# Kernel optimization log

Measured on AMD Instinct MI355X. Metric: run time of the kernel, lower is better.

## Reference

```python
import jax, jax.numpy as jnp
import numpy as np

BETA = 0.25
B, N, D = 8, 4096, 256
NUM_CODES = 4096


def setup_inputs() -> dict:
    key = jax.random.key(0)
    kx, kc = jax.random.split(key)
    x = jax.random.normal(kx, (B, N, D), dtype=jnp.float32)
    # matches nn.init.uniform_(weight, -1/dim, 1/dim)
    codebook = jax.random.uniform(kc, (NUM_CODES, D), dtype=jnp.float32,
                                  minval=-1.0 / D, maxval=1.0 / D)
    return {"x": x, "codebook": codebook}


def reference(x, codebook):
    b, n, d = x.shape
    flat = x.reshape(b * n, d)                                   # [BN, D]
    # squared euclidean distances: ||z||^2 - 2 z.e^T + ||e||^2   # [BN, K]
    distances = (jnp.sum(flat * flat, axis=1, keepdims=True)
                 - 2.0 * jnp.einsum('md,kd->mk', flat, codebook)
                 + jnp.sum(codebook * codebook, axis=1)[None, :])
    indices = jnp.argmin(distances, axis=1)                      # [BN]
    z_q = codebook[indices].reshape(b, n, d)                     # [B, N, D]
    # commitment + codebook losses (detach == stop_gradient)
    sg = jax.lax.stop_gradient
    loss = jnp.mean((sg(z_q) - x) ** 2) + BETA * jnp.mean((z_q - sg(x)) ** 2)
    # straight-through estimator
    z_q_st = x + sg(z_q - x)
    return z_q_st, loss, indices.reshape(b, n)
```

## Files before the change

kernel.cpp:

```cpp
#include <hip/hip_runtime.h>

#define MTOT 32768
#define KC   4096
#define DDIM 256
#define BM   128
#define ZELEMS (MTOT * DDIM)
#define THRESH 2.0e-4f
#define WLCAP 8192
#define RGRID 2048

typedef _Float16 half8 __attribute__((ext_vector_type(8)));
typedef float f32x4 __attribute__((ext_vector_type(4)));

__device__ __forceinline__ void gload_lds16(const void* g, void* l) {
  __builtin_amdgcn_global_load_lds(
      (const __attribute__((address_space(1))) void*)g,
      (__attribute__((address_space(3))) void*)l, 16, 0, 0);
}

__device__ __forceinline__ float sqr_rn(float v) { return __fmul_rn(v, v); }

__global__ __launch_bounds__(256) void vq_prep2(const float* __restrict__ x,
                                                const float* __restrict__ cb,
                                                float* __restrict__ S,
                                                float* __restrict__ cnorm,
                                                _Float16* __restrict__ cbsw,
                                                int* __restrict__ wl_count,
                                                double* __restrict__ accum) {
  const int t = threadIdx.x;
  if (blockIdx.x == 0 && t == 0) { *accum = 0.0; *wl_count = 0; }
  const int sub = t >> 4, lane16 = t & 15;
  const int h = lane16 >> 3, j = lane16 & 7;
  const bool isrow = blockIdx.x < 2048;
  const int idx = (isrow ? blockIdx.x : blockIdx.x - 2048) * 16 + sub;
  const float* p = (isrow ? x + (size_t)idx * DDIM : cb + (size_t)idx * DDIM);

  float r = 0.f;
  const float* q = p + h * 128 + j;
#pragma unroll
  for (int i = 0; i < 16; ++i) r = __fadd_rn(r, sqr_rn(q[i * 8]));
  r = __fadd_rn(r, __shfl_xor(r, 1, 64));
  r = __fadd_rn(r, __shfl_xor(r, 2, 64));
  r = __fadd_rn(r, __shfl_xor(r, 4, 64));
  float sv = __fadd_rn(r, __shfl_xor(r, 8, 64));
  if (lane16 == 0) {
    if (isrow) S[idx] = sv; else cnorm[idx] = sv;
  }

  if (!isrow) {
    const int sw = idx & 7;
    _Float16* dst = cbsw + (size_t)idx * DDIM;
#pragma unroll
    for (int c = 0; c < 2; ++c) {
      int jj = lane16 + c * 16;
      float4 a4 = *reinterpret_cast<const float4*>(p + jj * 8);
      float4 b4 = *reinterpret_cast<const float4*>(p + jj * 8 + 4);
      union { half8 v; _Float16 hh[8]; } u;
      u.hh[0] = (_Float16)(a4.x * 256.0f); u.hh[1] = (_Float16)(a4.y * 256.0f);
      u.hh[2] = (_Float16)(a4.z * 256.0f); u.hh[3] = (_Float16)(a4.w * 256.0f);
      u.hh[4] = (_Float16)(b4.x * 256.0f); u.hh[5] = (_Float16)(b4.y * 256.0f);
      u.hh[6] = (_Float16)(b4.z * 256.0f); u.hh[7] = (_Float16)(b4.w * 256.0f);
      *reinterpret_cast<half8*>(dst + ((jj ^ sw) * 8)) = u.v;
    }
  }
}

__global__ __launch_bounds__(512, 2) void vq_score(const float* __restrict__ x,
                                                   const _Float16* __restrict__ cbsw,
                                                   const float* __restrict__ Sarr,
                                                   const float* __restrict__ cnorm,
                                                   int* __restrict__ bestidx,
                                                   int* __restrict__ wl,
                                                   int* __restrict__ wl_count,
                                                   double* __restrict__ accum) {
  __shared__ _Float16 cbt[2][64 * DDIM];
  __shared__ float cn[KC];
  __shared__ float scrV1[4][BM];
  __shared__ float scrV2[4][BM];
  __shared__ int   scrI1[4][BM];
  __shared__ float wred[8];

  const int t = threadIdx.x;
  const int m0 = blockIdx.x * BM;
  const int lane = t & 63, w = t >> 6;
  const int rg = w >> 2, cg = w & 3;
  const int lo = lane & 15, hi = lane >> 4;

#pragma unroll
  for (int j = 0; j < 4; ++j)
    gload_lds16(cbsw + 0 * 16384 + w * 2048 + j * 512 + lane * 8,
                &cbt[0][w * 2048 + j * 512]);
#pragma unroll
  for (int j = 0; j < 4; ++j)
    gload_lds16(cbsw + 1 * 16384 + w * 2048 + j * 512 + lane * 8,
                &cbt[1][w * 2048 + j * 512]);

#pragma unroll
  for (int i = 0; i < 2; ++i) {
    int fi = t + i * 512;
    *reinterpret_cast<float4*>(&cn[fi * 4]) =
        *reinterpret_cast<const float4*>(cnorm + fi * 4);
  }

  half8 a[4][8];
#pragma unroll
  for (int s2 = 0; s2 < 4; ++s2) {
    const float* xr = x + (size_t)(m0 + rg * 64 + s2 * 16 + lo) * DDIM + hi * 8;
#pragma unroll
    for (int s = 0; s < 8; ++s) {
      float4 u0 = *reinterpret_cast<const float4*>(xr + s * 32);
      float4 u1 = *reinterpret_cast<const float4*>(xr + s * 32 + 4);
      union { half8 v; _Float16 h[8]; } uu;
      uu.h[0] = (_Float16)u0.x; uu.h[1] = (_Float16)u0.y;
      uu.h[2] = (_Float16)u0.z; uu.h[3] = (_Float16)u0.w;
      uu.h[4] = (_Float16)u1.x; uu.h[5] = (_Float16)u1.y;
      uu.h[6] = (_Float16)u1.z; uu.h[7] = (_Float16)u1.w;
      a[s2][s] = uu.v;
    }
  }

  const int code_l = cg * 16 + lo;
  const int bswz = (lo & 7) << 3;

  float v1[4][4], v2[4][4]; int i1[4][4];
#pragma unroll
  for (int s2 = 0; s2 < 4; ++s2)
#pragma unroll
    for (int r = 0; r < 4; ++r) { v1[s2][r] = 3.4e38f; v2[s2][r] = 3.4e38f; i1[s2][r] = 0; }

  __syncthreads();

  for (int kt = 0; kt < KC / 64; ++kt) {
    const int cur = kt & 1;
    if (kt < KC / 64 - 1) asm volatile("s_waitcnt vmcnt(4)" ::: "memory");
    else                  asm volatile("s_waitcnt vmcnt(0)" ::: "memory");
    __builtin_amdgcn_s_barrier();

    const float C = cn[kt * 64 + code_l];
    f32x4 acc[4];
#pragma unroll
    for (int s2 = 0; s2 < 4; ++s2) acc[s2] = (f32x4){0.f, 0.f, 0.f, 0.f};
#pragma unroll
    for (int s = 0; s < 8; ++s) {
      half8 b = *reinterpret_cast<half8*>(
          &cbt[cur][(code_l * DDIM + s * 32 + hi * 8) ^ bswz]);
      acc[0] = __builtin_amdgcn_mfma_f32_16x16x32_f16(a[0][s], b, acc[0], 0, 0, 0);
      acc[1] = __builtin_amdgcn_mfma_f32_16x16x32_f16(a[1][s], b, acc[1], 0, 0, 0);
      acc[2] = __builtin_amdgcn_mfma_f32_16x16x32_f16(a[2][s], b, acc[2], 0, 0, 0);
      acc[3] = __builtin_amdgcn_mfma_f32_16x16x32_f16(a[3][s], b, acc[3], 0, 0, 0);
    }
    const int code = kt * 64 + code_l;
#pragma unroll
    for (int s2 = 0; s2 < 4; ++s2) {
#pragma unroll
      for (int r = 0; r < 4; ++r) {
        float sv = fmaf(acc[s2][r], -0.0078125f, C);
        float mx = fmaxf(v1[s2][r], sv);
        v2[s2][r] = fminf(v2[s2][r], mx);
        bool lt = sv < v1[s2][r];
        if (lt) { v1[s2][r] = sv; i1[s2][r] = code; }
      }
    }

    __builtin_amdgcn_s_barrier();
    if (kt < KC / 64 - 2) {
#pragma unroll
      for (int j = 0; j < 4; ++j)
        gload_lds16(cbsw + (size_t)(kt + 2) * 16384 + w * 2048 + j * 512 + lane * 8,
                    &cbt[cur][w * 2048 + j * 512]);
    }
  }

#pragma unroll
  for (int s2 = 0; s2 < 4; ++s2) {
#pragma unroll
    for (int r = 0; r < 4; ++r) {
      float v = v1[s2][r], u = v2[s2][r]; int ii = i1[s2][r];
#pragma unroll
      for (int m = 1; m <= 8; m <<= 1) {
        float ov = __shfl_xor(v, m, 64);
        int   oi = __shfl_xor(ii, m, 64);
        float ou = __shfl_xor(u, m, 64);
        float mx = fmaxf(v, ov);
        u = fminf(fminf(u, ou), mx);
        bool take = (ov < v) || (ov == v && oi < ii);
        if (take) { v = ov; ii = oi; }
      }
      if (lo == 0) {
        int rowl = rg * 64 + s2 * 16 + hi * 4 + r;
        scrV1[cg][rowl] = v;
        scrV2[cg][rowl] = u;
        scrI1[cg][rowl] = ii;
      }
    }
  }
  __syncthreads();

  float part = 0.f;
  if (t < BM) {
    float bv1 = 3.4e38f, bv2 = 3.4e38f; int bi1 = 0x7fffffff;
#pragma unroll
    for (int c = 0; c < 4; ++c) {
      float v = scrV1[c][t];
      float u = scrV2[c][t];
      int  ii = scrI1[c][t];
      float mx = fmaxf(bv1, v);
      bv2 = fminf(fminf(bv2, u), mx);
      if (v < bv1 || (v == bv1 && ii < bi1)) { bv1 = v; bi1 = ii; }
    }
    int row = m0 + t;
    bestidx[row] = bi1;
    float gap = bv2 - bv1;
    if (gap <= THRESH) {
      int pos = atomicAdd(wl_count, 1);
      if (pos >= WLCAP) part = __fadd_rn(Sarr[row], bv1);
      else wl[pos] = row;
    } else {
      part = __fadd_rn(Sarr[row], bv1);
    }
  }
#pragma unroll
  for (int off = 32; off >= 1; off >>= 1) part += __shfl_down(part, off, 64);
  if (lane == 0) wred[w] = part;
  __syncthreads();
  if (t == 0) {
    double s = 0.0;
#pragma unroll
    for (int i = 0; i < 8; ++i) s += (double)wred[i];
    atomicAdd(accum, s);
  }
}

__global__ __launch_bounds__(256) void vq_rescore(const float* __restrict__ x,
                                                  const float* __restrict__ cb,
                                                  const float* __restrict__ Sarr,
                                                  const float* __restrict__ cnorm,
                                                  const int* __restrict__ wl,
                                                  const int* __restrict__ wl_count,
                                                  float* __restrict__ pD,
                                                  int* __restrict__ pI) {
  const int cnt = min(*wl_count, WLCAP);
  if (cnt == 0) return;
  const int ngroups = (cnt + 3) >> 2;
  const int nitems = ngroups * 16;

  __shared__ float xs[4][260];
  __shared__ int rsh[4];
  __shared__ float scrv[4][4];
  __shared__ int   scri[4][4];

  const int t = threadIdx.x;
  const int lane = t & 63, w = t >> 6;

  for (int item = blockIdx.x; item < nitems; item += RGRID) {
    const int g = item >> 4, chunk = item & 15;
    __syncthreads();
    if (t < 4) { int e = g * 4 + t; rsh[t] = wl[(e < cnt) ? e : g * 4]; }
    __syncthreads();
    { int i = t >> 6, dq = t & 63;
      *reinterpret_cast<float4*>(&xs[i][dq * 4]) =
          *reinterpret_cast<const float4*>(x + (size_t)rsh[i] * DDIM + dq * 4); }
    __syncthreads();

    const int code = chunk * 256 + t;
    const float* cp = cb + (size_t)code * DDIM;
    const float C = cnorm[code];

    float acc[4][4];
#pragma unroll
    for (int i = 0; i < 4; ++i)
#pragma unroll
      for (int l = 0; l < 4; ++l) acc[i][l] = 0.f;

#pragma unroll 8
    for (int dq = 0; dq < 64; ++dq) {
      float4 cv = *reinterpret_cast<const float4*>(cp + dq * 4);
#pragma unroll
      for (int i = 0; i < 4; ++i) {
        float4 xv = *reinterpret_cast<float4*>(&xs[i][dq * 4]);
        acc[i][0] = __fadd_rn(acc[i][0], __fmul_rn(xv.x, cv.x));
        acc[i][1] = __fadd_rn(acc[i][1], __fmul_rn(xv.y, cv.y));
        acc[i][2] = __fadd_rn(acc[i][2], __fmul_rn(xv.z, cv.z));
        acc[i][3] = __fadd_rn(acc[i][3], __fmul_rn(xv.w, cv.w));
      }
    }

#pragma unroll
    for (int i = 0; i < 4; ++i) {
      float e = __fadd_rn(__fadd_rn(acc[i][0], acc[i][1]),
                          __fadd_rn(acc[i][2], acc[i][3]));
      float Sv = Sarr[rsh[i]];
      float D = __fadd_rn(__fsub_rn(Sv, __fmul_rn(2.0f, e)), C);
      float v = D; int ii = code;
#pragma unroll
      for (int m = 1; m <= 32; m <<= 1) {
        float ov = __shfl_xor(v, m, 64);
        int   oi = __shfl_xor(ii, m, 64);
        if (ov < v || (ov == v && oi < ii)) { v = ov; ii = oi; }
      }
      if (lane == 0) { scrv[i][w] = v; scri[i][w] = ii; }
    }
    __syncthreads();
    if (t < 4) {
      float bv = 3.4e38f; int bi = 0x7fffffff;
#pragma unroll
      for (int c = 0; c < 4; ++c) {
        float v = scrv[t][c]; int ii = scri[t][c];
        if (v < bv || (v == bv && ii < bi)) { bv = v; bi = ii; }
      }
      int rpos = g * 4 + t;
      if (rpos < cnt) { pD[rpos * 16 + chunk] = bv; pI[rpos * 16 + chunk] = bi; }
    }
  }
}

__global__ __launch_bounds__(256) void vq_combine(const int* __restrict__ wl,
                                                  const int* __restrict__ wl_count,
                                                  const float* __restrict__ pD,
                                                  const int* __restrict__ pI,
                                                  int* __restrict__ bestidx,
                                                  double* __restrict__ accum) {
  const int cnt = min(*wl_count, WLCAP);
  for (int r = blockIdx.x * 256 + threadIdx.x; r < cnt; r += gridDim.x * 256) {
    float bv = 3.4e38f; int bi = 0x7fffffff;
#pragma unroll
    for (int c = 0; c < 16; ++c) {
      float v = pD[r * 16 + c]; int ii = pI[r * 16 + c];
      if (v < bv || (v == bv && ii < bi)) { bv = v; bi = ii; }
    }
    bestidx[wl[r]] = bi;
    atomicAdd(accum, (double)bv);
  }
}

__global__ __launch_bounds__(256) void vq_emit(const float* __restrict__ x,
                                               const float* __restrict__ cb,
                                               const int* __restrict__ bestidx,
                                               float* __restrict__ out) {
  __shared__ int ish[64];
  const int t = threadIdx.x;
  const int m0 = blockIdx.x * 64;
  if (t < 64) {
    int ii = bestidx[m0 + t];
    ish[t] = ii;
    out[(size_t)ZELEMS + 1 + m0 + t] = (float)ii;
  }
  __syncthreads();
#pragma unroll
  for (int i = 0; i < 16; ++i) {
    int fi = t + i * 256;
    int row = fi >> 6, dc = fi & 63;
    int code = ish[row];
    float4 c4 = *reinterpret_cast<const float4*>(cb + (size_t)code * DDIM + dc * 4);
    float4 x4 = *reinterpret_cast<const float4*>(x + (size_t)(m0 + row) * DDIM + dc * 4);
    float4 o;
    o.x = __fadd_rn(x4.x, __fsub_rn(c4.x, x4.x));
    o.y = __fadd_rn(x4.y, __fsub_rn(c4.y, x4.y));
    o.z = __fadd_rn(x4.z, __fsub_rn(c4.z, x4.z));
    o.w = __fadd_rn(x4.w, __fsub_rn(c4.w, x4.w));
    *reinterpret_cast<float4*>(out + (size_t)(m0 + row) * DDIM + dc * 4) = o;
  }
}

__global__ void vq_final(const double* __restrict__ accum, float* __restrict__ out) {
  out[ZELEMS] = (float)(1.25 * accum[0] / (double)ZELEMS);
}

extern "C" void kernel_launch(void* const* d_in, const int* in_sizes, int n_in,
                              void* d_out, int out_size, void* d_ws, size_t ws_size,
                              hipStream_t stream) {
  const float* x  = (const float*)d_in[0];
  const float* cb = (const float*)d_in[1];
  float* out = (float*)d_out;

  char* ws = (char*)d_ws;
  float*     S        = (float*)(ws + 0);
  float*     cnorm    = (float*)(ws + 131072);
  int*       bestidx  = (int*)  (ws + 147456);
  int*       wl       = (int*)  (ws + 278528);
  int*       wl_count = (int*)  (ws + 311296);
  double*    accum    = (double*)(ws + 311312);
  float*     pD       = (float*)(ws + 315392);
  int*       pI       = (int*)  (ws + 839680);
  _Float16*  cbsw     = (_Float16*)(ws + 1363968);

  vq_prep2<<<2304, 256, 0, stream>>>(x, cb, S, cnorm, cbsw, wl_count, accum);
  vq_score<<<MTOT / BM, 512, 0, stream>>>(x, cbsw, S, cnorm, bestidx, wl, wl_count, accum);
  vq_rescore<<<RGRID, 256, 0, stream>>>(x, cb, S, cnorm, wl, wl_count, pD, pI);
  vq_combine<<<8, 256, 0, stream>>>(wl, wl_count, pD, pI, bestidx, accum);
  vq_emit<<<MTOT / 64, 256, 0, stream>>>(x, cb, bestidx, out);
  vq_final<<<1, 1, 0, stream>>>(accum, out);
}
```

Baseline: 176.8 us.

## Deepen codebook LDS pipeline to four buffers, two tiles per barrier

```diff
diff --git a/kernel.cpp b/kernel.cpp
--- a/kernel.cpp
+++ b/kernel.cpp
@@ -65,7 +65,7 @@
   }
 }
 
-__global__ __launch_bounds__(512, 2) void vq_score(const float* __restrict__ x,
+__global__ __launch_bounds__(512, 1) void vq_score(const float* __restrict__ x,
                                                    const _Float16* __restrict__ cbsw,
                                                    const float* __restrict__ Sarr,
                                                    const float* __restrict__ cnorm,
@@ -73,7 +73,7 @@
                                                    int* __restrict__ wl,
                                                    int* __restrict__ wl_count,
                                                    double* __restrict__ accum) {
-  __shared__ _Float16 cbt[2][64 * DDIM];
+  __shared__ _Float16 cbt[4][64 * DDIM];
   __shared__ float cn[KC];
   __shared__ float scrV1[4][BM];
   __shared__ float scrV2[4][BM];
@@ -87,13 +87,11 @@
   const int lo = lane & 15, hi = lane >> 4;
 
 #pragma unroll
-  for (int j = 0; j < 4; ++j)
-    gload_lds16(cbsw + 0 * 16384 + w * 2048 + j * 512 + lane * 8,
-                &cbt[0][w * 2048 + j * 512]);
-#pragma unroll
-  for (int j = 0; j < 4; ++j)
-    gload_lds16(cbsw + 1 * 16384 + w * 2048 + j * 512 + lane * 8,
-                &cbt[1][w * 2048 + j * 512]);
+  for (int T = 0; T < 4; ++T)
+#pragma unroll
+    for (int j = 0; j < 4; ++j)
+      gload_lds16(cbsw + (size_t)T * 16384 + w * 2048 + j * 512 + lane * 8,
+                  &cbt[T][w * 2048 + j * 512]);
 
 #pragma unroll
   for (int i = 0; i < 2; ++i) {
@@ -130,46 +128,60 @@
 
   __syncthreads();
 
-  for (int kt = 0; kt < KC / 64; ++kt) {
-    const int cur = kt & 1;
-    if (kt < KC / 64 - 1) asm volatile("s_waitcnt vmcnt(4)" ::: "memory");
-    else                  asm volatile("s_waitcnt vmcnt(0)" ::: "memory");
+#define TILE_BODY(buf, ktc)                                                          \
+  do {                                                                               \
+    const float C = cn[(ktc) * 64 + code_l];                                         \
+    f32x4 acc[4];                                                                    \
+    _Pragma("unroll")                                                                \
+    for (int s2 = 0; s2 < 4; ++s2) acc[s2] = (f32x4){0.f, 0.f, 0.f, 0.f};            \
+    __builtin_amdgcn_s_setprio(1);                                                   \
+    _Pragma("unroll")                                                                \
+    for (int s = 0; s < 8; ++s) {                                                    \
+      half8 b = *reinterpret_cast<half8*>(                                           \
+          &cbt[buf][(code_l * DDIM + s * 32 + hi * 8) ^ bswz]);                      \
+      acc[0] = __builtin_amdgcn_mfma_f32_16x16x32_f16(a[0][s], b, acc[0], 0, 0, 0);  \
+      acc[1] = __builtin_amdgcn_mfma_f32_16x16x32_f16(a[1][s], b, acc[1], 0, 0, 0);  \
+      acc[2] = __builtin_amdgcn_mfma_f32_16x16x32_f16(a[2][s], b, acc[2], 0, 0, 0);  \
+      acc[3] = __builtin_amdgcn_mfma_f32_16x16x32_f16(a[3][s], b, acc[3], 0, 0, 0);  \
+    }                                                                                \
+    __builtin_amdgcn_s_setprio(0);                                                   \
+    const int code = (ktc) * 64 + code_l;                                            \
+    _Pragma("unroll")                                                                \
+    for (int s2 = 0; s2 < 4; ++s2) {                                                 \
+      _Pragma("unroll")                                                              \
+      for (int r = 0; r < 4; ++r) {                                                  \
+        float sv = fmaf(acc[s2][r], -0.0078125f, C);     \
+        float mx = fmaxf(v1[s2][r], sv);                                             \
+        v2[s2][r] = fminf(v2[s2][r], mx);                                            \
+        bool lt = sv < v1[s2][r];                                                    \
+        if (lt) { v1[s2][r] = sv; i1[s2][r] = code; }                                \
+      }                                                                              \
+    }                                                                                \
+  } while (0)
+
+  for (int p = 0; p < 32; ++p) {
+    const int t0 = 2 * p, t1 = 2 * p + 1;
+    const int b0 = t0 & 3, b1 = t1 & 3;
+    if (p < 31) asm volatile("s_waitcnt vmcnt(8)" ::: "memory");
+    else        asm volatile("s_waitcnt vmcnt(0)" ::: "memory");
     __builtin_amdgcn_s_barrier();
 
-    const float C = cn[kt * 64 + code_l];
-    f32x4 acc[4];
-#pragma unroll
-    for (int s2 = 0; s2 < 4; ++s2) acc[s2] = (f32x4){0.f, 0.f, 0.f, 0.f};
-#pragma unroll
-    for (int s = 0; s < 8; ++s) {
-      half8 b = *reinterpret_cast<half8*>(
-          &cbt[cur][(code_l * DDIM + s * 32 + hi * 8) ^ bswz]);
-      acc[0] = __builtin_amdgcn_mfma_f32_16x16x32_f16(a[0][s], b, acc[0], 0, 0, 0);
-      acc[1] = __builtin_amdgcn_mfma_f32_16x16x32_f16(a[1][s], b, acc[1], 0, 0, 0);
-      acc[2] = __builtin_amdgcn_mfma_f32_16x16x32_f16(a[2][s], b, acc[2], 0, 0, 0);
-      acc[3] = __builtin_amdgcn_mfma_f32_16x16x32_f16(a[3][s], b, acc[3], 0, 0, 0);
-    }
-    const int code = kt * 64 + code_l;
-#pragma unroll
-    for (int s2 = 0; s2 < 4; ++s2) {
-#pragma unroll
-      for (int r = 0; r < 4; ++r) {
-        float sv = fmaf(acc[s2][r], -0.0078125f, C);
-        float mx = fmaxf(v1[s2][r], sv);
-        v2[s2][r] = fminf(v2[s2][r], mx);
-        bool lt = sv < v1[s2][r];
-        if (lt) { v1[s2][r] = sv; i1[s2][r] = code; }
-      }
-    }
+    TILE_BODY(b0, t0);
+    TILE_BODY(b1, t1);
 
     __builtin_amdgcn_s_barrier();
-    if (kt < KC / 64 - 2) {
+    if (2 * p + 4 < 64) {
 #pragma unroll
       for (int j = 0; j < 4; ++j)
-        gload_lds16(cbsw + (size_t)(kt + 2) * 16384 + w * 2048 + j * 512 + lane * 8,
-                    &cbt[cur][w * 2048 + j * 512]);
-    }
-  }
+        gload_lds16(cbsw + (size_t)(2 * p + 4) * 16384 + w * 2048 + j * 512 + lane * 8,
+                    &cbt[b0][w * 2048 + j * 512]);
+#pragma unroll
+      for (int j = 0; j < 4; ++j)
+        gload_lds16(cbsw + (size_t)(2 * p + 5) * 16384 + w * 2048 + j * 512 + lane * 8,
+                    &cbt[b1][w * 2048 + j * 512]);
+    }
+  }
+#undef TILE_BODY
 
 #pragma unroll
   for (int s2 = 0; s2 < 4; ++s2) {
```

Result: slower. 183.9 us (+4.0%).

## Fuse output emission into scoring kernel and patch rescored rows in combine

Applied to the files above, without the earlier changes.

```diff
diff --git a/kernel.cpp b/kernel.cpp
--- a/kernel.cpp
+++ b/kernel.cpp
@@ -66,18 +66,20 @@
 }
 
 __global__ __launch_bounds__(512, 2) void vq_score(const float* __restrict__ x,
+                                                   const float* __restrict__ cbf,
                                                    const _Float16* __restrict__ cbsw,
                                                    const float* __restrict__ Sarr,
                                                    const float* __restrict__ cnorm,
-                                                   int* __restrict__ bestidx,
                                                    int* __restrict__ wl,
                                                    int* __restrict__ wl_count,
-                                                   double* __restrict__ accum) {
+                                                   double* __restrict__ accum,
+                                                   float* __restrict__ out) {
   __shared__ _Float16 cbt[2][64 * DDIM];
   __shared__ float cn[KC];
   __shared__ float scrV1[4][BM];
   __shared__ float scrV2[4][BM];
   __shared__ int   scrI1[4][BM];
+  __shared__ int   idx_sh[BM];
   __shared__ float wred[8];
 
   const int t = threadIdx.x;
@@ -209,7 +211,8 @@
       if (v < bv1 || (v == bv1 && ii < bi1)) { bv1 = v; bi1 = ii; }
     }
     int row = m0 + t;
-    bestidx[row] = bi1;
+    idx_sh[t] = bi1;
+    out[(size_t)ZELEMS + 1 + row] = (float)bi1;
     float gap = bv2 - bv1;
     if (gap <= THRESH) {
       int pos = atomicAdd(wl_count, 1);
@@ -228,6 +231,21 @@
 #pragma unroll
     for (int i = 0; i < 8; ++i) s += (double)wred[i];
     atomicAdd(accum, s);
+  }
+
+#pragma unroll
+  for (int i = 0; i < 16; ++i) {
+    int fi = t + i * 512;
+    int row = fi >> 6, dc = fi & 63;
+    int code = idx_sh[row];
+    float4 c4 = *reinterpret_cast<const float4*>(cbf + (size_t)code * DDIM + dc * 4);
+    float4 x4 = *reinterpret_cast<const float4*>(x + (size_t)(m0 + row) * DDIM + dc * 4);
+    float4 o;
+    o.x = __fadd_rn(x4.x, __fsub_rn(c4.x, x4.x));
+    o.y = __fadd_rn(x4.y, __fsub_rn(c4.y, x4.y));
+    o.z = __fadd_rn(x4.z, __fsub_rn(c4.z, x4.z));
+    o.w = __fadd_rn(x4.w, __fsub_rn(c4.w, x4.w));
+    *reinterpret_cast<float4*>(out + (size_t)(m0 + row) * DDIM + dc * 4) = o;
   }
 }
 
@@ -241,13 +259,13 @@
                                                   int* __restrict__ pI) {
   const int cnt = min(*wl_count, WLCAP);
   if (cnt == 0) return;
-  const int ngroups = (cnt + 3) >> 2;
+  const int ngroups = (cnt + 7) >> 3;
   const int nitems = ngroups * 16;
 
-  __shared__ float xs[4][260];
-  __shared__ int rsh[4];
-  __shared__ float scrv[4][4];
-  __shared__ int   scri[4][4];
+  __shared__ float xs[8][260];
+  __shared__ int rsh[8];
+  __shared__ float scrv[8][4];
+  __shared__ int   scri[8][4];
 
   const int t = threadIdx.x;
   const int lane = t & 63, w = t >> 6;
@@ -255,28 +273,31 @@
   for (int item = blockIdx.x; item < nitems; item += RGRID) {
     const int g = item >> 4, chunk = item & 15;
     __syncthreads();
-    if (t < 4) { int e = g * 4 + t; rsh[t] = wl[(e < cnt) ? e : g * 4]; }
+    if (t < 8) { int e = g * 8 + t; rsh[t] = wl[(e < cnt) ? e : g * 8]; }
     __syncthreads();
-    { int i = t >> 6, dq = t & 63;
+#pragma unroll
+    for (int j = 0; j < 2; ++j) {
+      int fi = t + j * 256, i = fi >> 6, dq = fi & 63;
       *reinterpret_cast<float4*>(&xs[i][dq * 4]) =
-          *reinterpret_cast<const float4*>(x + (size_t)rsh[i] * DDIM + dq * 4); }
+          *reinterpret_cast<const float4*>(x + (size_t)rsh[i] * DDIM + dq * 4);
+    }
     __syncthreads();
 
     const int code = chunk * 256 + t;
     const float* cp = cb + (size_t)code * DDIM;
     const float C = cnorm[code];
 
-    float acc[4][4];
-#pragma unroll
-    for (int i = 0; i < 4; ++i)
+    float acc[8][4];
+#pragma unroll
+    for (int i = 0; i < 8; ++i)
 #pragma unroll
       for (int l = 0; l < 4; ++l) acc[i][l] = 0.f;
 
-#pragma unroll 8
+#pragma unroll 4
     for (int dq = 0; dq < 64; ++dq) {
       float4 cv = *reinterpret_cast<const float4*>(cp + dq * 4);
 #pragma unroll
-      for (int i = 0; i < 4; ++i) {
+      for (int i = 0; i < 8; ++i) {
         float4 xv = *reinterpret_cast<float4*>(&xs[i][dq * 4]);
         acc[i][0] = __fadd_rn(acc[i][0], __fmul_rn(xv.x, cv.x));
         acc[i][1] = __fadd_rn(acc[i][1], __fmul_rn(xv.y, cv.y));
@@ -286,7 +307,7 @@
     }
 
 #pragma unroll
-    for (int i = 0; i < 4; ++i) {
+    for (int i = 0; i < 8; ++i) {
       float e = __fadd_rn(__fadd_rn(acc[i][0], acc[i][1]),
                           __fadd_rn(acc[i][2], acc[i][3]));
       float Sv = Sarr[rsh[i]];
@@ -301,69 +322,66 @@
       if (lane == 0) { scrv[i][w] = v; scri[i][w] = ii; }
     }
     __syncthreads();
-    if (t < 4) {
+    if (t < 8) {
       float bv = 3.4e38f; int bi = 0x7fffffff;
 #pragma unroll
       for (int c = 0; c < 4; ++c) {
         float v = scrv[t][c]; int ii = scri[t][c];
         if (v < bv || (v == bv && ii < bi)) { bv = v; bi = ii; }
       }
-      int rpos = g * 4 + t;
+      int rpos = g * 8 + t;
       if (rpos < cnt) { pD[rpos * 16 + chunk] = bv; pI[rpos * 16 + chunk] = bi; }
     }
   }
 }
 
-__global__ __launch_bounds__(256) void vq_combine(const int* __restrict__ wl,
-                                                  const int* __restrict__ wl_count,
-                                                  const float* __restrict__ pD,
-                                                  const int* __restrict__ pI,
-                                                  int* __restrict__ bestidx,
-                                                  double* __restrict__ accum) {
+__global__ __launch_bounds__(256) void vq_combine2(const float* __restrict__ x,
+                                                   const float* __restrict__ cb,
+                                                   const int* __restrict__ wl,
+                                                   const int* __restrict__ wl_count,
+                                                   const float* __restrict__ pD,
+                                                   const int* __restrict__ pI,
+                                                   float* __restrict__ out,
+                                                   double* __restrict__ accum) {
+  __shared__ int fixi[WLCAP];
+  __shared__ double dred[4];
   const int cnt = min(*wl_count, WLCAP);
-  for (int r = blockIdx.x * 256 + threadIdx.x; r < cnt; r += gridDim.x * 256) {
+  const int t = threadIdx.x;
+
+  double s = 0.0;
+  for (int r = t; r < cnt; r += 256) {
     float bv = 3.4e38f; int bi = 0x7fffffff;
 #pragma unroll
     for (int c = 0; c < 16; ++c) {
       float v = pD[r * 16 + c]; int ii = pI[r * 16 + c];
       if (v < bv || (v == bv && ii < bi)) { bv = v; bi = ii; }
     }
-    bestidx[wl[r]] = bi;
-    atomicAdd(accum, (double)bv);
-  }
-}
-
-__global__ __launch_bounds__(256) void vq_emit(const float* __restrict__ x,
-                                               const float* __restrict__ cb,
-                                               const int* __restrict__ bestidx,
-                                               float* __restrict__ out) {
-  __shared__ int ish[64];
-  const int t = threadIdx.x;
-  const int m0 = blockIdx.x * 64;
-  if (t < 64) {
-    int ii = bestidx[m0 + t];
-    ish[t] = ii;
-    out[(size_t)ZELEMS + 1 + m0 + t] = (float)ii;
-  }
+    fixi[r] = bi;
+    out[(size_t)ZELEMS + 1 + wl[r]] = (float)bi;
+    s += (double)bv;
+  }
+#pragma unroll
+  for (int off = 32; off >= 1; off >>= 1) s += __shfl_down(s, off, 64);
+  if ((t & 63) == 0) dred[t >> 6] = s;
   __syncthreads();
-#pragma unroll
-  for (int i = 0; i < 16; ++i) {
-    int fi = t + i * 256;
-    int row = fi >> 6, dc = fi & 63;
-    int code = ish[row];
+  if (t == 0) {
+    double tot = (dred[0] + dred[1]) + (dred[2] + dred[3]);
+    double prev = atomicAdd(accum, tot);
+    out[ZELEMS] = (float)(1.25 * (prev + tot) / (double)ZELEMS);
+  }
+
+  for (int f = t; f < cnt * 64; f += 256) {
+    int r = f >> 6, dc = f & 63;
+    int row = wl[r], code = fixi[r];
     float4 c4 = *reinterpret_cast<const float4*>(cb + (size_t)code * DDIM + dc * 4);
-    float4 x4 = *reinterpret_cast<const float4*>(x + (size_t)(m0 + row) * DDIM + dc * 4);
+    float4 x4 = *reinterpret_cast<const float4*>(x + (size_t)row * DDIM + dc * 4);
     float4 o;
     o.x = __fadd_rn(x4.x, __fsub_rn(c4.x, x4.x));
     o.y = __fadd_rn(x4.y, __fsub_rn(c4.y, x4.y));
     o.z = __fadd_rn(x4.z, __fsub_rn(c4.z, x4.z));
     o.w = __fadd_rn(x4.w, __fsub_rn(c4.w, x4.w));
-    *reinterpret_cast<float4*>(out + (size_t)(m0 + row) * DDIM + dc * 4) = o;
-  }
-}
-
-__global__ void vq_final(const double* __restrict__ accum, float* __restrict__ out) {
-  out[ZELEMS] = (float)(1.25 * accum[0] / (double)ZELEMS);
+    *reinterpret_cast<float4*>(out + (size_t)row * DDIM + dc * 4) = o;
+  }
 }
 
 extern "C" void kernel_launch(void* const* d_in, const int* in_sizes, int n_in,
@@ -376,7 +394,6 @@
   char* ws = (char*)d_ws;
   float*     S        = (float*)(ws + 0);
   float*     cnorm    = (float*)(ws + 131072);
-  int*       bestidx  = (int*)  (ws + 147456);
   int*       wl       = (int*)  (ws + 278528);
   int*       wl_count = (int*)  (ws + 311296);
   double*    accum    = (double*)(ws + 311312);
@@ -385,9 +402,7 @@
   _Float16*  cbsw     = (_Float16*)(ws + 1363968);
 
   vq_prep2<<<2304, 256, 0, stream>>>(x, cb, S, cnorm, cbsw, wl_count, accum);
-  vq_score<<<MTOT / BM, 512, 0, stream>>>(x, cbsw, S, cnorm, bestidx, wl, wl_count, accum);
+  vq_score<<<MTOT / BM, 512, 0, stream>>>(x, cb, cbsw, S, cnorm, wl, wl_count, accum, out);
   vq_rescore<<<RGRID, 256, 0, stream>>>(x, cb, S, cnorm, wl, wl_count, pD, pI);
-  vq_combine<<<8, 256, 0, stream>>>(wl, wl_count, pD, pI, bestidx, accum);
-  vq_emit<<<MTOT / 64, 256, 0, stream>>>(x, cb, bestidx, out);
-  vq_final<<<1, 1, 0, stream>>>(accum, out);
-}
+  vq_combine2<<<1, 256, 0, stream>>>(x, cb, wl, wl_count, pD, pI, out, accum);
+}
```

Result: slower. 189.6 us (+7.3%).
